# Performance work log

Measured on AMD Instinct MI355X. Metric: run time of the kernel, lower is better.

Reference implementation:

```python
import jax, jax.numpy as jnp
import numpy as np

TEMPERATURE = 0.07
MASK_VAL = -9e15
EPS = 1e-8

def setup_inputs() -> dict:
    key = jax.random.key(0)
    features = jax.random.normal(key, (8192, 256), dtype=jnp.float32)
    return {"features": features}

def reference(features):
    # features: [N, D]
    N = features.shape[0]
    norm = jnp.linalg.norm(features, axis=-1, keepdims=True)
    f = features / jnp.maximum(norm, EPS)
    # cosine similarity via GEMM: [N, N]
    sim = f @ f.T
    idx = jnp.arange(N)
    # mask self-similarity BEFORE temperature scaling (as in the torch code)
    sim = jnp.where(idx[:, None] == idx[None, :], MASK_VAL, sim)
    sim = sim / TEMPERATURE
    # positive of row i is column (i - N//2) mod N (eye rolled by N//2 along dim 0)
    pos_col = (idx - N // 2) % N
    pos = sim[idx, pos_col]
    nll = -pos + jax.nn.logsumexp(sim, axis=-1)
    return nll.mean()
```

## Files before the change

### kernel.cpp

```cpp
#include <hip/hip_runtime.h>
#include <hip/hip_bf16.h>
#include <math.h>

#define N_ROWS 8192
#define D_DIM  256
#define HALF_N 4096
#define INV_T      14.285714285714286f
#define SCALE_LOG2 20.609929155556620f
#define NEG_SCALE  -20.609929155556620f
#define EPSV   1e-8f

typedef __attribute__((ext_vector_type(8))) short bf16x8;
typedef __attribute__((ext_vector_type(4))) float f32x4;

#define AS1 __attribute__((address_space(1)))
#define AS3 __attribute__((address_space(3)))

__device__ inline unsigned short f2bf(float x) {
    unsigned int u = __float_as_uint(x);
    unsigned int r = (u + 0x7fffu + ((u >> 16) & 1u)) >> 16;
    return (unsigned short)r;
}

__global__ __launch_bounds__(256) void k_norm(const float* __restrict__ feat,
                                              unsigned short* __restrict__ fbf,
                                              float* __restrict__ sumexp,
                                              float* __restrict__ out) {
    const int tid = threadIdx.x;
    const int gid = blockIdx.x * 256 + tid;
    if (gid < N_ROWS) sumexp[gid] = 0.f;
    if (gid == 0) out[0] = 0.f;

    const int w = tid >> 6, lane = tid & 63;
    const int row = blockIdx.x * 4 + w;
    const float4 v = ((const float4*)(feat + row * D_DIM))[lane];
    float ss = v.x*v.x + v.y*v.y + v.z*v.z + v.w*v.w;
    #pragma unroll
    for (int off = 32; off; off >>= 1) ss += __shfl_xor(ss, off);
    const float scale = 1.f / fmaxf(sqrtf(ss), EPSV);
    ushort4 o;
    o.x = f2bf(v.x * scale);
    o.y = f2bf(v.y * scale);
    o.z = f2bf(v.z * scale);
    o.w = f2bf(v.w * scale);
    ((ushort4*)(fbf + row * D_DIM))[lane] = o;
}

__global__ __launch_bounds__(256, 2) void k_sim(const unsigned short* __restrict__ fbf,
                                                float* __restrict__ sumexp) {
    __shared__ __align__(16) char Bs[16384];
    const int tid  = threadIdx.x;
    const int lane = tid & 63;
    const int w    = tid >> 6;
    const int q    = lane >> 4, l15 = lane & 15;

    const int bid = blockIdx.x;
    int rt = (int)((sqrtf(8.f * (float)bid + 1.f) - 1.f) * 0.5f);
    while ((rt + 1) * (rt + 2) / 2 <= bid) ++rt;
    while (rt * (rt + 1) / 2 > bid) --rt;
    const int cs = bid - rt * (rt + 1) / 2;
    const bool isDiag = (rt == cs);

    const int rowBase = rt * 256 + w * 64;
    const char* Bgbase = (const char*)fbf + (size_t)(cs * 256) * (D_DIM * 2);

    #pragma unroll
    for (int i = 0; i < 4; ++i) {
        const int idx = i * 256 + tid;
        const int col = idx >> 5;
        const int cir = idx & 31;
        __builtin_amdgcn_global_load_lds(
            (const AS1 void*)(Bgbase + col * 512 + ((cir ^ (col & 7)) << 4)),
            (AS3 void*)(Bs + idx * 16), 16, 0, 0);
    }

    bf16x8 afrag[8][4];
    #pragma unroll
    for (int t = 0; t < 8; ++t)
        #pragma unroll
        for (int ri = 0; ri < 4; ++ri)
            afrag[t][ri] = *(const bf16x8*)(fbf + (rowBase + ri*16 + l15) * D_DIM
                                                + t*32 + q*8);

    float rsum[4][4];
    #pragma unroll
    for (int ri = 0; ri < 4; ++ri)
        #pragma unroll
        for (int r = 0; r < 4; ++r) rsum[ri][r] = 0.f;

    #pragma unroll 1
    for (int jt = 0; jt < 8; ++jt) {
        const int colBase = cs * 256 + jt * 32;

        __syncthreads();

        f32x4 acc[4][2];
        #pragma unroll
        for (int ri = 0; ri < 4; ++ri)
            #pragma unroll
            for (int ci = 0; ci < 2; ++ci) acc[ri][ci] = (f32x4){0.f, 0.f, 0.f, 0.f};

        #pragma unroll
        for (int t = 0; t < 8; ++t) {
            bf16x8 bfrag[2];
            #pragma unroll
            for (int ci = 0; ci < 2; ++ci) {
                const int c   = ci * 16 + l15;
                const int cir = t * 4 + q;
                bfrag[ci] = *(const bf16x8*)(Bs + c * 512 + ((cir ^ (c & 7)) << 4));
            }
            #pragma unroll
            for (int ri = 0; ri < 4; ++ri)
                #pragma unroll
                for (int ci = 0; ci < 2; ++ci)
                    acc[ri][ci] = __builtin_amdgcn_mfma_f32_16x16x32_bf16(
                        afrag[t][ri], bfrag[ci], acc[ri][ci], 0, 0, 0);
        }

        if (jt < 7) {
            __syncthreads();
            const char* Bg = Bgbase + (size_t)(jt + 1) * (32 * 512);
            #pragma unroll
            for (int i = 0; i < 4; ++i) {
                const int idx = i * 256 + tid;
                const int col = idx >> 5;
                const int cir = idx & 31;
                __builtin_amdgcn_global_load_lds(
                    (const AS1 void*)(Bg + col * 512 + ((cir ^ (col & 7)) << 4)),
                    (AS3 void*)(Bs + idx * 16), 16, 0, 0);
            }
        }

        if (isDiag) {
            #pragma unroll
            for (int ri = 0; ri < 4; ++ri) {
                const int trow = rowBase + ri * 16;
                #pragma unroll
                for (int ci = 0; ci < 2; ++ci) {
                    const int tcol = colBase + ci * 16;
                    if (trow == tcol) {
                        #pragma unroll
                        for (int r = 0; r < 4; ++r) {
                            const float e = __builtin_amdgcn_exp2f(
                                __builtin_fmaf(acc[ri][ci][r], SCALE_LOG2, NEG_SCALE));
                            rsum[ri][r] += (q * 4 + r == l15) ? 0.f : e;
                        }
                    } else {
                        #pragma unroll
                        for (int r = 0; r < 4; ++r)
                            rsum[ri][r] += __builtin_amdgcn_exp2f(
                                __builtin_fmaf(acc[ri][ci][r], SCALE_LOG2, NEG_SCALE));
                    }
                }
            }
        } else {
            float csum0 = 0.f, csum1 = 0.f;
            #pragma unroll
            for (int ri = 0; ri < 4; ++ri) {
                #pragma unroll
                for (int r = 0; r < 4; ++r) {
                    const float e0 = __builtin_amdgcn_exp2f(
                        __builtin_fmaf(acc[ri][0][r], SCALE_LOG2, NEG_SCALE));
                    const float e1 = __builtin_amdgcn_exp2f(
                        __builtin_fmaf(acc[ri][1][r], SCALE_LOG2, NEG_SCALE));
                    rsum[ri][r] += e0 + e1;
                    csum0 += e0;
                    csum1 += e1;
                }
            }
            csum0 += __shfl_xor(csum0, 16); csum0 += __shfl_xor(csum0, 32);
            csum1 += __shfl_xor(csum1, 16); csum1 += __shfl_xor(csum1, 32);
            if (q == 0)      atomicAdd(&sumexp[colBase      + l15], csum0);
            else if (q == 1) atomicAdd(&sumexp[colBase + 16 + l15], csum1);
        }
    }

    #pragma unroll
    for (int ri = 0; ri < 4; ++ri)
        #pragma unroll
        for (int r = 0; r < 4; ++r) {
            float s = rsum[ri][r];
            s += __shfl_xor(s, 1);
            s += __shfl_xor(s, 2);
            s += __shfl_xor(s, 4);
            s += __shfl_xor(s, 8);
            if (l15 == 0)
                atomicAdd(&sumexp[rowBase + ri * 16 + q * 4 + r], s);
        }
}

__global__ __launch_bounds__(256) void k_nll(const float* __restrict__ feat,
                                             const float* __restrict__ sumexp,
                                             float* __restrict__ out) {
    __shared__ float red[4];
    const int tid = threadIdx.x, w = tid >> 6, lane = tid & 63;
    const int i  = blockIdx.x * 4 + w;
    const int pc = (i + HALF_N) & (N_ROWS - 1);
    const float4 a = ((const float4*)(feat + i  * D_DIM))[lane];
    const float4 b = ((const float4*)(feat + pc * D_DIM))[lane];
    float dab = a.x*b.x + a.y*b.y + a.z*b.z + a.w*b.w;
    float daa = a.x*a.x + a.y*a.y + a.z*a.z + a.w*a.w;
    float dbb = b.x*b.x + b.y*b.y + b.z*b.z + b.w*b.w;
    #pragma unroll
    for (int off = 32; off; off >>= 1) {
        dab += __shfl_xor(dab, off);
        daa += __shfl_xor(daa, off);
        dbb += __shfl_xor(dbb, off);
    }
    if (lane == 0) {
        const float pos = dab / (fmaxf(sqrtf(daa), EPSV) * fmaxf(sqrtf(dbb), EPSV));
        red[w] = INV_T + logf(sumexp[i]) - pos * INV_T;
    }
    __syncthreads();
    if (tid == 0)
        atomicAdd(out, (red[0] + red[1] + red[2] + red[3]) * (1.f / N_ROWS));
}

extern "C" void kernel_launch(void* const* d_in, const int* in_sizes, int n_in,
                              void* d_out, int out_size, void* d_ws, size_t ws_size,
                              hipStream_t stream) {
    const float* feat = (const float*)d_in[0];
    char* ws = (char*)d_ws;
    unsigned short* fbf = (unsigned short*)ws;
    float* sumexp = (float*)(ws + 4u * 1024u * 1024u);

    k_norm<<<N_ROWS / 4, 256, 0, stream>>>(feat, fbf, sumexp, (float*)d_out);
    k_sim <<<528,        256, 0, stream>>>(fbf, sumexp);
    k_nll <<<N_ROWS / 4, 256, 0, stream>>>(feat, sumexp, (float*)d_out);
}
```

Baseline: 125.0 us.

## Balance triangular sim work across 512 blocks via flattened 32-column chunk ranges

Flattens the 528 triangular 256x256 tiles into 4224 column chunks of 32 and gives each of 512 blocks a contiguous range of about 8.25 chunks, crossing tile boundaries as needed. A's fragments are reloaded and the row sums flushed whenever a block moves to a new tile. This targets the tail imbalance of 528 blocks on 256 CUs at 2 blocks per CU, which leaves a second partial wave. The cost is extra A reloads, extra atomics at tile boundaries, and more control flow inside the loop.

```diff
diff --git a/kernel.cpp b/kernel.cpp
--- a/kernel.cpp
+++ b/kernel.cpp
@@ -54,43 +54,72 @@
     const int w    = tid >> 6;
     const int q    = lane >> 4, l15 = lane & 15;
 
-    const int bid = blockIdx.x;
-    int rt = (int)((sqrtf(8.f * (float)bid + 1.f) - 1.f) * 0.5f);
-    while ((rt + 1) * (rt + 2) / 2 <= bid) ++rt;
-    while (rt * (rt + 1) / 2 > bid) --rt;
-    const int cs = bid - rt * (rt + 1) / 2;
-    const bool isDiag = (rt == cs);
-
-    const int rowBase = rt * 256 + w * 64;
-    const char* Bgbase = (const char*)fbf + (size_t)(cs * 256) * (D_DIM * 2);
-
-    #pragma unroll
-    for (int i = 0; i < 4; ++i) {
-        const int idx = i * 256 + tid;
-        const int col = idx >> 5;
-        const int cir = idx & 31;
-        __builtin_amdgcn_global_load_lds(
-            (const AS1 void*)(Bgbase + col * 512 + ((cir ^ (col & 7)) << 4)),
-            (AS3 void*)(Bs + idx * 16), 16, 0, 0);
-    }
+    int g          = (33 * blockIdx.x) >> 2;
+    const int gEnd = (33 * (blockIdx.x + 1)) >> 2;
+
+    const int tt0 = g >> 3;
+    int rt = (int)((sqrtf(8.f * (float)tt0 + 1.f) - 1.f) * 0.5f);
+    while ((rt + 1) * (rt + 2) / 2 <= tt0) ++rt;
+    while (rt * (rt + 1) / 2 > tt0) --rt;
+    int cs = tt0 - rt * (rt + 1) / 2;
+    int jt = g & 7;
+
+#define STAGE(colRow0) do {                                                   \
+        const char* Bg_ = (const char*)fbf + (size_t)(colRow0) * 512;         \
+        _Pragma("unroll")                                                     \
+        for (int i_ = 0; i_ < 4; ++i_) {                                      \
+            const int idx_ = i_ * 256 + tid;                                  \
+            const int col_ = idx_ >> 5;                                       \
+            const int cir_ = idx_ & 31;                                       \
+            __builtin_amdgcn_global_load_lds(                                 \
+                (const AS1 void*)(Bg_ + col_ * 512 + ((cir_ ^ (col_ & 7)) << 4)), \
+                (AS3 void*)(Bs + idx_ * 16), 16, 0, 0);                       \
+        }                                                                     \
+    } while (0)
 
     bf16x8 afrag[8][4];
-    #pragma unroll
-    for (int t = 0; t < 8; ++t)
-        #pragma unroll
-        for (int ri = 0; ri < 4; ++ri)
-            afrag[t][ri] = *(const bf16x8*)(fbf + (rowBase + ri*16 + l15) * D_DIM
-                                                + t*32 + q*8);
+#define LOAD_A(rt_) do {                                                      \
+        const int rowBase_ = (rt_) * 256 + w * 64;                            \
+        _Pragma("unroll")                                                     \
+        for (int t_ = 0; t_ < 8; ++t_)                                        \
+            _Pragma("unroll")                                                 \
+            for (int ri_ = 0; ri_ < 4; ++ri_)                                 \
+                afrag[t_][ri_] = *(const bf16x8*)(fbf                         \
+                    + (rowBase_ + ri_*16 + l15) * D_DIM + t_*32 + q*8);       \
+    } while (0)
 
     float rsum[4][4];
-    #pragma unroll
-    for (int ri = 0; ri < 4; ++ri)
-        #pragma unroll
-        for (int r = 0; r < 4; ++r) rsum[ri][r] = 0.f;
-
-    #pragma unroll 1
-    for (int jt = 0; jt < 8; ++jt) {
+#define ZERO_RSUM() do {                                                      \
+        _Pragma("unroll")                                                     \
+        for (int ri_ = 0; ri_ < 4; ++ri_)                                     \
+            _Pragma("unroll")                                                 \
+            for (int r_ = 0; r_ < 4; ++r_) rsum[ri_][r_] = 0.f;               \
+    } while (0)
+
+#define FLUSH_RSUM(rt_) do {                                                  \
+        const int rowBase_ = (rt_) * 256 + w * 64;                            \
+        _Pragma("unroll")                                                     \
+        for (int ri_ = 0; ri_ < 4; ++ri_)                                     \
+            _Pragma("unroll")                                                 \
+            for (int r_ = 0; r_ < 4; ++r_) {                                  \
+                float s_ = rsum[ri_][r_];                                     \
+                s_ += __shfl_xor(s_, 1);                                      \
+                s_ += __shfl_xor(s_, 2);                                      \
+                s_ += __shfl_xor(s_, 4);                                      \
+                s_ += __shfl_xor(s_, 8);                                      \
+                if (l15 == 0)                                                 \
+                    atomicAdd(&sumexp[rowBase_ + ri_ * 16 + q * 4 + r_], s_); \
+            }                                                                 \
+    } while (0)
+
+    STAGE(cs * 256 + jt * 32);
+    LOAD_A(rt);
+    ZERO_RSUM();
+
+    while (true) {
         const int colBase = cs * 256 + jt * 32;
+        const bool isDiag = (rt == cs);
+        const int rowBase = rt * 256 + w * 64;
 
         __syncthreads();
 
@@ -117,18 +146,17 @@
                         afrag[t][ri], bfrag[ci], acc[ri][ci], 0, 0, 0);
         }
 
-        if (jt < 7) {
+        const bool more = (g + 1 < gEnd);
+        int nrt = rt, ncs = cs, njt = jt + 1;
+        if (njt == 8) {
+            njt = 0; ncs = cs + 1;
+            if (ncs > rt) { nrt = rt + 1; ncs = 0; }
+        }
+
+        if (more) {
             __syncthreads();
-            const char* Bg = Bgbase + (size_t)(jt + 1) * (32 * 512);
-            #pragma unroll
-            for (int i = 0; i < 4; ++i) {
-                const int idx = i * 256 + tid;
-                const int col = idx >> 5;
-                const int cir = idx & 31;
-                __builtin_amdgcn_global_load_lds(
-                    (const AS1 void*)(Bg + col * 512 + ((cir ^ (col & 7)) << 4)),
-                    (AS3 void*)(Bs + idx * 16), 16, 0, 0);
-            }
+            STAGE(ncs * 256 + njt * 32);
+            if (njt == 0) LOAD_A(nrt);
         }
 
         if (isDiag) {
@@ -173,20 +201,20 @@
             if (q == 0)      atomicAdd(&sumexp[colBase      + l15], csum0);
             else if (q == 1) atomicAdd(&sumexp[colBase + 16 + l15], csum1);
         }
+
+        if (!more) break;
+        if (njt == 0) {
+            FLUSH_RSUM(rt);
+            ZERO_RSUM();
+        }
+        rt = nrt; cs = ncs; jt = njt; ++g;
     }
 
-    #pragma unroll
-    for (int ri = 0; ri < 4; ++ri)
-        #pragma unroll
-        for (int r = 0; r < 4; ++r) {
-            float s = rsum[ri][r];
-            s += __shfl_xor(s, 1);
-            s += __shfl_xor(s, 2);
-            s += __shfl_xor(s, 4);
-            s += __shfl_xor(s, 8);
-            if (l15 == 0)
-                atomicAdd(&sumexp[rowBase + ri * 16 + q * 4 + r], s);
-        }
+    FLUSH_RSUM(rt);
+#undef STAGE
+#undef LOAD_A
+#undef ZERO_RSUM
+#undef FLUSH_RSUM
 }
 
 __global__ __launch_bounds__(256) void k_nll(const float* __restrict__ feat,
@@ -225,6 +253,6 @@
     float* sumexp = (float*)(ws + 4u * 1024u * 1024u);
 
     k_norm<<<N_ROWS / 4, 256, 0, stream>>>(feat, fbf, sumexp, (float*)d_out);
-    k_sim <<<528,        256, 0, stream>>>(fbf, sumexp);
+    k_sim <<<512,        256, 0, stream>>>(fbf, sumexp);
     k_nll <<<N_ROWS / 4, 256, 0, stream>>>(feat, sumexp, (float*)d_out);
 }
```

Measured after the change: 124.2 us. Within noise of the previous version (-0.6%).
